# Kernel tuning notes

Hardware: AMD Instinct MI355X
Metric: run time of the kernel (lower is better)

The kernel has to match this reference:

```python
import jax, jax.numpy as jnp
import numpy as np
import math

B, H, N, D = 4, 8, 2048, 64


def setup_inputs() -> dict:
    key = jax.random.key(0)
    kq, kk, kv = jax.random.split(key, 3)
    q = jax.random.normal(kq, (B, H, N, D), dtype=jnp.float32)
    k = jax.random.normal(kk, (B, H, N, D), dtype=jnp.float32)
    v = jax.random.normal(kv, (B, H, N, D), dtype=jnp.float32)
    return {"q": q, "k": k, "v": v}


def reference(q, k, v):
    # global_attention_Sub: expanded squared L2 distance ||q_i - k_j||^2
    # = qq_i - 2 q_i.k_j + kk_j, then softmax(-dist/sqrt(D)) @ v.
    scale = math.sqrt(q.shape[-1])
    inner = -2.0 * jnp.einsum('bhnd,bhmd->bhnm', q, k)          # [B,H,N,N]
    qq = jnp.sum(q * q, axis=-1, keepdims=True)                  # [B,H,N,1]
    kk = jnp.sum(k * k, axis=-1, keepdims=True)                  # [B,H,N,1]
    diff_sq = qq + inner + jnp.swapaxes(kk, -1, -2)              # [B,H,N,N]
    attn = jax.nn.softmax(-diff_sq / scale, axis=-1)
    x = jnp.einsum('bhnm,bhmd->bhnd', attn, v)                   # [B,H,N,D]
    return jnp.transpose(x, (0, 2, 1, 3))                        # [B,N,H,D]
```

## Files before the change

### kernel.cpp

```cpp
#include <hip/hip_runtime.h>

typedef __bf16 bf16x4 __attribute__((ext_vector_type(4)));
typedef __bf16 bf16x8 __attribute__((ext_vector_type(8)));
typedef float floatx4 __attribute__((ext_vector_type(4)));

constexpr int Bc = 4, Hc = 8, Nc = 2048, Dc = 64;
constexpr int BQ = 128;
constexpr int WQ = 32;
constexpr int TK = 64;
constexpr int SKS = 72;
constexpr int SPS = 72;

__global__ __launch_bounds__(256, 2) void attn_dist_kernel(
    const float* __restrict__ Qg, const float* __restrict__ Kg,
    const float* __restrict__ Vg, float* __restrict__ Og)
{
    __shared__ __align__(16) __bf16 sK[TK * SKS];
    __shared__ __align__(16) __bf16 sV[Dc * 64];
    __shared__ __align__(16) __bf16 sP[BQ * SPS];
    __shared__ __align__(16) float  skk[TK];
    __shared__ __align__(16) float  sl[BQ];

    const int tid  = threadIdx.x;
    const int wave = tid >> 6;
    const int lane = tid & 63;
    const int qd   = lane >> 4;
    const int c    = lane & 15;

    const int qt = blockIdx.x;
    const int bh = blockIdx.y;
    const size_t base = (size_t)bh * Nc * Dc;
    const float* Qp = Qg + base;
    const float* Kp = Kg + base;
    const float* Vp = Vg + base;

    constexpr float LOG2E = 1.44269504088896340736f;
    const float qscale  = 0.25f  * LOG2E;
    const float kkscale = 0.125f * LOG2E;

    const int i0 = qt * BQ + wave * WQ;

    bf16x8 qf[2][2];
#pragma unroll
    for (int h = 0; h < 2; ++h) {
        const float* qrow = Qp + (size_t)(i0 + h * 16 + c) * Dc + qd * 8;
#pragma unroll
        for (int ks = 0; ks < 2; ++ks) {
            float4 a = *(const float4*)(qrow + ks * 32);
            float4 b = *(const float4*)(qrow + ks * 32 + 4);
            bf16x8 f;
            f[0] = (__bf16)(a.x * qscale); f[1] = (__bf16)(a.y * qscale);
            f[2] = (__bf16)(a.z * qscale); f[3] = (__bf16)(a.w * qscale);
            f[4] = (__bf16)(b.x * qscale); f[5] = (__bf16)(b.y * qscale);
            f[6] = (__bf16)(b.z * qscale); f[7] = (__bf16)(b.w * qscale);
            qf[h][ks] = f;
        }
    }

    const int js  = tid >> 2;
    const int ds_ = (tid & 3) * 16;

    float4 kreg[4], vreg[4];
    {
        const float* kr = Kp + (size_t)js * Dc + ds_;
        const float* vr = Vp + (size_t)js * Dc + ds_;
#pragma unroll
        for (int m = 0; m < 4; ++m) {
            kreg[m] = *(const float4*)(kr + m * 4);
            vreg[m] = *(const float4*)(vr + m * 4);
        }
    }

    floatx4 oacc[2][4];
#pragma unroll
    for (int h = 0; h < 2; ++h)
#pragma unroll
        for (int dt = 0; dt < 4; ++dt)
#pragma unroll
            for (int e = 0; e < 4; ++e) oacc[h][dt][e] = 0.f;
    float lp[2] = {0.f, 0.f};

    for (int jt = 0; jt < Nc / TK; ++jt) {
        __syncthreads();
        {
            float ss = 0.f;
#pragma unroll
            for (int m = 0; m < 4; ++m)
                ss += kreg[m].x * kreg[m].x + kreg[m].y * kreg[m].y
                    + kreg[m].z * kreg[m].z + kreg[m].w * kreg[m].w;
            ss += __shfl_xor(ss, 1);
            ss += __shfl_xor(ss, 2);
            if ((tid & 3) == 0) skk[js] = ss * kkscale;

            bf16x8 kb0, kb1;
            kb0[0]=(__bf16)kreg[0].x; kb0[1]=(__bf16)kreg[0].y;
            kb0[2]=(__bf16)kreg[0].z; kb0[3]=(__bf16)kreg[0].w;
            kb0[4]=(__bf16)kreg[1].x; kb0[5]=(__bf16)kreg[1].y;
            kb0[6]=(__bf16)kreg[1].z; kb0[7]=(__bf16)kreg[1].w;
            kb1[0]=(__bf16)kreg[2].x; kb1[1]=(__bf16)kreg[2].y;
            kb1[2]=(__bf16)kreg[2].z; kb1[3]=(__bf16)kreg[2].w;
            kb1[4]=(__bf16)kreg[3].x; kb1[5]=(__bf16)kreg[3].y;
            kb1[6]=(__bf16)kreg[3].z; kb1[7]=(__bf16)kreg[3].w;
            *(bf16x8*)&sK[js * SKS + ds_]     = kb0;
            *(bf16x8*)&sK[js * SKS + ds_ + 8] = kb1;

            float vv[16];
#pragma unroll
            for (int m = 0; m < 4; ++m) {
                vv[4*m+0] = vreg[m].x; vv[4*m+1] = vreg[m].y;
                vv[4*m+2] = vreg[m].z; vv[4*m+3] = vreg[m].w;
            }
            const int jc = js >> 3, jo = js & 7;
#pragma unroll
            for (int e = 0; e < 16; ++e) {
                const int d = ds_ + e;
                const int f = (d ^ (d >> 3)) & 7;
                sV[d * 64 + ((jc ^ f) << 3) + jo] = (__bf16)vv[e];
            }
        }
        __syncthreads();

        if (jt + 1 < Nc / TK) {
            const float* kr = Kp + (size_t)((jt + 1) * TK + js) * Dc + ds_;
            const float* vr = Vp + (size_t)((jt + 1) * TK + js) * Dc + ds_;
#pragma unroll
            for (int m = 0; m < 4; ++m) {
                kreg[m] = *(const float4*)(kr + m * 4);
                vreg[m] = *(const float4*)(vr + m * 4);
            }
        }

        floatx4 st[2][4];
#pragma unroll
        for (int kt = 0; kt < 4; ++kt) {
            floatx4 kkf = *(const floatx4*)&skk[kt * 16 + qd * 4];
#pragma unroll
            for (int r = 0; r < 4; ++r) { st[0][kt][r] = -kkf[r]; st[1][kt][r] = -kkf[r]; }
        }
#pragma unroll
        for (int kt = 0; kt < 4; ++kt)
#pragma unroll
            for (int ks = 0; ks < 2; ++ks) {
                bf16x8 kf = *(const bf16x8*)&sK[(kt * 16 + c) * SKS + ks * 32 + qd * 8];
                st[0][kt] = __builtin_amdgcn_mfma_f32_16x16x32_bf16(kf, qf[0][ks], st[0][kt], 0, 0, 0);
                st[1][kt] = __builtin_amdgcn_mfma_f32_16x16x32_bf16(kf, qf[1][ks], st[1][kt], 0, 0, 0);
            }

#pragma unroll
        for (int h = 0; h < 2; ++h) {
            const int prow = wave * WQ + h * 16 + c;
#pragma unroll
            for (int kt = 0; kt < 4; ++kt) {
                float p0 = __builtin_amdgcn_exp2f(st[h][kt][0]);
                float p1 = __builtin_amdgcn_exp2f(st[h][kt][1]);
                float p2 = __builtin_amdgcn_exp2f(st[h][kt][2]);
                float p3 = __builtin_amdgcn_exp2f(st[h][kt][3]);
                lp[h] += (p0 + p1) + (p2 + p3);
                bf16x4 pk;
                pk[0]=(__bf16)p0; pk[1]=(__bf16)p1; pk[2]=(__bf16)p2; pk[3]=(__bf16)p3;
                *(bf16x4*)&sP[prow * SPS + kt * 16 + qd * 4] = pk;
            }
        }

        bf16x8 pf[2][2];
#pragma unroll
        for (int h = 0; h < 2; ++h)
#pragma unroll
            for (int ks = 0; ks < 2; ++ks)
                pf[h][ks] = *(const bf16x8*)&sP[(wave * WQ + h * 16 + c) * SPS + ks * 32 + qd * 8];

#pragma unroll
        for (int dt = 0; dt < 4; ++dt) {
            const int d = dt * 16 + c;
            const int f = (d ^ (d >> 3)) & 7;
#pragma unroll
            for (int ks = 0; ks < 2; ++ks) {
                bf16x8 vf = *(const bf16x8*)&sV[d * 64 + (((ks * 4 + qd) ^ f) << 3)];
                oacc[0][dt] = __builtin_amdgcn_mfma_f32_16x16x32_bf16(pf[0][ks], vf, oacc[0][dt], 0, 0, 0);
                oacc[1][dt] = __builtin_amdgcn_mfma_f32_16x16x32_bf16(pf[1][ks], vf, oacc[1][dt], 0, 0, 0);
            }
        }
    }

#pragma unroll
    for (int h = 0; h < 2; ++h) {
        float l = lp[h];
        l += __shfl_xor(l, 16);
        l += __shfl_xor(l, 32);
        if (qd == 0) sl[wave * WQ + h * 16 + c] = l;
    }
    const int b = bh >> 3, hh = bh & 7;
#pragma unroll
    for (int h = 0; h < 2; ++h) {
        floatx4 lf = *(const floatx4*)&sl[wave * WQ + h * 16 + qd * 4];
#pragma unroll
        for (int r = 0; r < 4; ++r) {
            const float inv = 1.f / lf[r];
            const int i = i0 + h * 16 + qd * 4 + r;
            float* orow = Og + (((size_t)b * Nc + i) * Hc + hh) * Dc + c;
#pragma unroll
            for (int dt = 0; dt < 4; ++dt)
                orow[dt * 16] = oacc[h][dt][r] * inv;
        }
    }
}

extern "C" void kernel_launch(void* const* d_in, const int* in_sizes, int n_in,
                              void* d_out, int out_size, void* d_ws, size_t ws_size,
                              hipStream_t stream) {
    const float* q = (const float*)d_in[0];
    const float* k = (const float*)d_in[1];
    const float* v = (const float*)d_in[2];
    float* out = (float*)d_out;
    dim3 grid(Nc / BQ, Bc * Hc);
    dim3 block(256);
    attn_dist_kernel<<<grid, block, 0, stream>>>(q, k, v, out);
}
```

Before: 147.6 us.

## Precompute swizzled bf16 K/V tiles in workspace and stream them via global_load_lds

A prep kernel converts K and V once to bf16 and writes pre-swizzled tiles to the workspace: K in row-major swizzled form, V transposed. It also stores the negated, scaled squared K norms. The attention kernel then double-buffers tiles into LDS with direct global-to-LDS DMA and needs one barrier per iteration instead of two. This removes the per-block conversion, norm computation and scattered LDS stores that every query tile repeated. In exchange it adds a second launch and a workspace write/read pass, and relies on the async DMA being complete at the barrier.

```diff
diff --git a/kernel.cpp b/kernel.cpp
--- a/kernel.cpp
+++ b/kernel.cpp
@@ -8,17 +8,88 @@
 constexpr int BQ = 128;
 constexpr int WQ = 32;
 constexpr int TK = 64;
-constexpr int SKS = 72;
+constexpr int NT = Nc / TK;
 constexpr int SPS = 72;
-
-__global__ __launch_bounds__(256, 2) void attn_dist_kernel(
-    const float* __restrict__ Qg, const float* __restrict__ Kg,
-    const float* __restrict__ Vg, float* __restrict__ Og)
+constexpr float LOG2E = 1.44269504088896340736f;
+
+constexpr size_t KSW_OFF = 0;
+constexpr size_t VSW_OFF = (size_t)32 * NT * 8192;
+constexpr size_t KKN_OFF = VSW_OFF * 2;
+
+typedef __attribute__((address_space(1))) const unsigned int gu32;
+typedef __attribute__((address_space(3))) unsigned int lu32;
+__device__ __forceinline__ void dma16(const void* g, void* l) {
+    __builtin_amdgcn_global_load_lds((gu32*)g, (lu32*)l, 16, 0, 0);
+}
+__device__ __forceinline__ void dma4(const void* g, void* l) {
+    __builtin_amdgcn_global_load_lds((gu32*)g, (lu32*)l, 4, 0, 0);
+}
+
+__global__ __launch_bounds__(256) void prep_kernel(
+    const float* __restrict__ Kg, const float* __restrict__ Vg, char* __restrict__ ws)
 {
-    __shared__ __align__(16) __bf16 sK[TK * SKS];
-    __shared__ __align__(16) __bf16 sV[Dc * 64];
+    __shared__ float sT[64 * 68];
+    const int tid = threadIdx.x;
+    const int jt = blockIdx.x, bh = blockIdx.y;
+    const int js = tid >> 2, dc = tid & 3, ds_ = dc * 16;
+
+    __bf16* Ksw = (__bf16*)(ws + KSW_OFF);
+    __bf16* Vsw = (__bf16*)(ws + VSW_OFF);
+    float*  kkn = (float*)(ws + KKN_OFF);
+    const size_t rb = ((size_t)bh * Nc + jt * 64 + js) * Dc + ds_;
+
+    {
+        float4 a0 = *(const float4*)(Kg + rb);
+        float4 a1 = *(const float4*)(Kg + rb + 4);
+        float4 a2 = *(const float4*)(Kg + rb + 8);
+        float4 a3 = *(const float4*)(Kg + rb + 12);
+        float ss = a0.x*a0.x + a0.y*a0.y + a0.z*a0.z + a0.w*a0.w
+                 + a1.x*a1.x + a1.y*a1.y + a1.z*a1.z + a1.w*a1.w
+                 + a2.x*a2.x + a2.y*a2.y + a2.z*a2.z + a2.w*a2.w
+                 + a3.x*a3.x + a3.y*a3.y + a3.z*a3.z + a3.w*a3.w;
+        ss += __shfl_xor(ss, 1);
+        ss += __shfl_xor(ss, 2);
+        if (dc == 0) kkn[(size_t)bh * Nc + jt * 64 + js] = -(ss * 0.125f * LOG2E);
+        bf16x8 c0, c1;
+        c0[0]=(__bf16)a0.x; c0[1]=(__bf16)a0.y; c0[2]=(__bf16)a0.z; c0[3]=(__bf16)a0.w;
+        c0[4]=(__bf16)a1.x; c0[5]=(__bf16)a1.y; c0[6]=(__bf16)a1.z; c0[7]=(__bf16)a1.w;
+        c1[0]=(__bf16)a2.x; c1[1]=(__bf16)a2.y; c1[2]=(__bf16)a2.z; c1[3]=(__bf16)a2.w;
+        c1[4]=(__bf16)a3.x; c1[5]=(__bf16)a3.y; c1[6]=(__bf16)a3.z; c1[7]=(__bf16)a3.w;
+        __bf16* tile = Ksw + ((size_t)bh * NT + jt) * 4096;
+        *(bf16x8*)(tile + (js * 8 + ((dc * 2    ) ^ (js & 7))) * 8) = c0;
+        *(bf16x8*)(tile + (js * 8 + ((dc * 2 + 1) ^ (js & 7))) * 8) = c1;
+    }
+    {
+        float4 v0 = *(const float4*)(Vg + rb);
+        float4 v1 = *(const float4*)(Vg + rb + 4);
+        float4 v2 = *(const float4*)(Vg + rb + 8);
+        float4 v3 = *(const float4*)(Vg + rb + 12);
+        float* r = &sT[js * 68 + ds_];
+        *(float4*)r = v0; *(float4*)(r + 4) = v1;
+        *(float4*)(r + 8) = v2; *(float4*)(r + 12) = v3;
+    }
+    __syncthreads();
+    {
+        const int d = tid >> 2;
+        __bf16* tile = Vsw + ((size_t)bh * NT + jt) * 4096;
+#pragma unroll
+        for (int e2 = 0; e2 < 2; ++e2) {
+            const int kc = (tid & 3) * 2 + e2;
+            bf16x8 cc;
+#pragma unroll
+            for (int e = 0; e < 8; ++e) cc[e] = (__bf16)sT[(kc * 8 + e) * 68 + d];
+            *(bf16x8*)(tile + (d * 8 + (kc ^ (d & 7))) * 8) = cc;
+        }
+    }
+}
+
+__global__ __launch_bounds__(256, 2) void attn_kernel(
+    const float* __restrict__ Qg, const char* __restrict__ ws, float* __restrict__ Og)
+{
+    __shared__ __align__(16) __bf16 sK[2][4096];
+    __shared__ __align__(16) __bf16 sV[2][4096];
+    __shared__ __align__(16) float  skk[2][64];
     __shared__ __align__(16) __bf16 sP[BQ * SPS];
-    __shared__ __align__(16) float  skk[TK];
     __shared__ __align__(16) float  sl[BQ];
 
     const int tid  = threadIdx.x;
@@ -29,21 +100,18 @@
 
     const int qt = blockIdx.x;
     const int bh = blockIdx.y;
-    const size_t base = (size_t)bh * Nc * Dc;
-    const float* Qp = Qg + base;
-    const float* Kp = Kg + base;
-    const float* Vp = Vg + base;
-
-    constexpr float LOG2E = 1.44269504088896340736f;
-    const float qscale  = 0.25f  * LOG2E;
-    const float kkscale = 0.125f * LOG2E;
-
+
+    const char* Kimg = ws + KSW_OFF + (size_t)bh * NT * 8192;
+    const char* Vimg = ws + VSW_OFF + (size_t)bh * NT * 8192;
+    const float* kkp = (const float*)(ws + KKN_OFF) + (size_t)bh * Nc;
+
+    const float qscale = 0.25f * LOG2E;
     const int i0 = qt * BQ + wave * WQ;
 
     bf16x8 qf[2][2];
 #pragma unroll
     for (int h = 0; h < 2; ++h) {
-        const float* qrow = Qp + (size_t)(i0 + h * 16 + c) * Dc + qd * 8;
+        const float* qrow = Qg + ((size_t)bh * Nc + i0 + h * 16 + c) * Dc + qd * 8;
 #pragma unroll
         for (int ks = 0; ks < 2; ++ks) {
             float4 a = *(const float4*)(qrow + ks * 32);
@@ -57,19 +125,8 @@
         }
     }
 
-    const int js  = tid >> 2;
-    const int ds_ = (tid & 3) * 16;
-
-    float4 kreg[4], vreg[4];
-    {
-        const float* kr = Kp + (size_t)js * Dc + ds_;
-        const float* vr = Vp + (size_t)js * Dc + ds_;
-#pragma unroll
-        for (int m = 0; m < 4; ++m) {
-            kreg[m] = *(const float4*)(kr + m * 4);
-            vreg[m] = *(const float4*)(vr + m * 4);
-        }
-    }
+    const int koff0 = c * 64 + ((qd ^ (c & 7)) << 3);
+    const int koff1 = c * 64 + (((4 + qd) ^ (c & 7)) << 3);
 
     floatx4 oacc[2][4];
 #pragma unroll
@@ -80,71 +137,42 @@
             for (int e = 0; e < 4; ++e) oacc[h][dt][e] = 0.f;
     float lp[2] = {0.f, 0.f};
 
-    for (int jt = 0; jt < Nc / TK; ++jt) {
+    auto stage = [&](int jt, int b) {
+        const char* ki = Kimg + (size_t)jt * 8192;
+        const char* vi = Vimg + (size_t)jt * 8192;
+#pragma unroll
+        for (int i = 0; i < 2; ++i) {
+            const int off    = wave * 2048 + i * 1024 + lane * 16;
+            const int ldsoff = wave * 2048 + i * 1024;
+            dma16(ki + off, (char*)&sK[b][0] + ldsoff);
+            dma16(vi + off, (char*)&sV[b][0] + ldsoff);
+        }
+        if (wave == 3) dma4(kkp + jt * 64 + lane, &skk[b][0]);
+    };
+
+    stage(0, 0);
+
+    for (int jt = 0; jt < NT; ++jt) {
+        const int b = jt & 1;
         __syncthreads();
-        {
-            float ss = 0.f;
-#pragma unroll
-            for (int m = 0; m < 4; ++m)
-                ss += kreg[m].x * kreg[m].x + kreg[m].y * kreg[m].y
-                    + kreg[m].z * kreg[m].z + kreg[m].w * kreg[m].w;
-            ss += __shfl_xor(ss, 1);
-            ss += __shfl_xor(ss, 2);
-            if ((tid & 3) == 0) skk[js] = ss * kkscale;
-
-            bf16x8 kb0, kb1;
-            kb0[0]=(__bf16)kreg[0].x; kb0[1]=(__bf16)kreg[0].y;
-            kb0[2]=(__bf16)kreg[0].z; kb0[3]=(__bf16)kreg[0].w;
-            kb0[4]=(__bf16)kreg[1].x; kb0[5]=(__bf16)kreg[1].y;
-            kb0[6]=(__bf16)kreg[1].z; kb0[7]=(__bf16)kreg[1].w;
-            kb1[0]=(__bf16)kreg[2].x; kb1[1]=(__bf16)kreg[2].y;
-            kb1[2]=(__bf16)kreg[2].z; kb1[3]=(__bf16)kreg[2].w;
-            kb1[4]=(__bf16)kreg[3].x; kb1[5]=(__bf16)kreg[3].y;
-            kb1[6]=(__bf16)kreg[3].z; kb1[7]=(__bf16)kreg[3].w;
-            *(bf16x8*)&sK[js * SKS + ds_]     = kb0;
-            *(bf16x8*)&sK[js * SKS + ds_ + 8] = kb1;
-
-            float vv[16];
-#pragma unroll
-            for (int m = 0; m < 4; ++m) {
-                vv[4*m+0] = vreg[m].x; vv[4*m+1] = vreg[m].y;
-                vv[4*m+2] = vreg[m].z; vv[4*m+3] = vreg[m].w;
-            }
-            const int jc = js >> 3, jo = js & 7;
-#pragma unroll
-            for (int e = 0; e < 16; ++e) {
-                const int d = ds_ + e;
-                const int f = (d ^ (d >> 3)) & 7;
-                sV[d * 64 + ((jc ^ f) << 3) + jo] = (__bf16)vv[e];
-            }
-        }
-        __syncthreads();
-
-        if (jt + 1 < Nc / TK) {
-            const float* kr = Kp + (size_t)((jt + 1) * TK + js) * Dc + ds_;
-            const float* vr = Vp + (size_t)((jt + 1) * TK + js) * Dc + ds_;
-#pragma unroll
-            for (int m = 0; m < 4; ++m) {
-                kreg[m] = *(const float4*)(kr + m * 4);
-                vreg[m] = *(const float4*)(vr + m * 4);
-            }
-        }
+        if (jt + 1 < NT) stage(jt + 1, b ^ 1);
 
         floatx4 st[2][4];
 #pragma unroll
         for (int kt = 0; kt < 4; ++kt) {
-            floatx4 kkf = *(const floatx4*)&skk[kt * 16 + qd * 4];
-#pragma unroll
-            for (int r = 0; r < 4; ++r) { st[0][kt][r] = -kkf[r]; st[1][kt][r] = -kkf[r]; }
-        }
-#pragma unroll
-        for (int kt = 0; kt < 4; ++kt)
-#pragma unroll
-            for (int ks = 0; ks < 2; ++ks) {
-                bf16x8 kf = *(const bf16x8*)&sK[(kt * 16 + c) * SKS + ks * 32 + qd * 8];
-                st[0][kt] = __builtin_amdgcn_mfma_f32_16x16x32_bf16(kf, qf[0][ks], st[0][kt], 0, 0, 0);
-                st[1][kt] = __builtin_amdgcn_mfma_f32_16x16x32_bf16(kf, qf[1][ks], st[1][kt], 0, 0, 0);
-            }
+            floatx4 kkf = *(const floatx4*)&skk[b][kt * 16 + qd * 4];
+            st[0][kt] = kkf; st[1][kt] = kkf;
+        }
+#pragma unroll
+        for (int kt = 0; kt < 4; ++kt) {
+            const __bf16* kbase = &sK[b][kt * 1024];
+            bf16x8 kf0 = *(const bf16x8*)(kbase + koff0);
+            bf16x8 kf1 = *(const bf16x8*)(kbase + koff1);
+            st[0][kt] = __builtin_amdgcn_mfma_f32_16x16x32_bf16(kf0, qf[0][0], st[0][kt], 0, 0, 0);
+            st[0][kt] = __builtin_amdgcn_mfma_f32_16x16x32_bf16(kf1, qf[0][1], st[0][kt], 0, 0, 0);
+            st[1][kt] = __builtin_amdgcn_mfma_f32_16x16x32_bf16(kf0, qf[1][0], st[1][kt], 0, 0, 0);
+            st[1][kt] = __builtin_amdgcn_mfma_f32_16x16x32_bf16(kf1, qf[1][1], st[1][kt], 0, 0, 0);
+        }
 
 #pragma unroll
         for (int h = 0; h < 2; ++h) {
@@ -157,11 +185,11 @@
                 float p3 = __builtin_amdgcn_exp2f(st[h][kt][3]);
                 lp[h] += (p0 + p1) + (p2 + p3);
                 bf16x4 pk;
-                pk[0]=(__bf16)p0; pk[1]=(__bf16)p1; pk[2]=(__bf16)p2; pk[3]=(__bf16)p3;
+                pk[0] = (__bf16)p0; pk[1] = (__bf16)p1;
+                pk[2] = (__bf16)p2; pk[3] = (__bf16)p3;
                 *(bf16x4*)&sP[prow * SPS + kt * 16 + qd * 4] = pk;
             }
         }
-
         bf16x8 pf[2][2];
 #pragma unroll
         for (int h = 0; h < 2; ++h)
@@ -171,14 +199,13 @@
 
 #pragma unroll
         for (int dt = 0; dt < 4; ++dt) {
-            const int d = dt * 16 + c;
-            const int f = (d ^ (d >> 3)) & 7;
-#pragma unroll
-            for (int ks = 0; ks < 2; ++ks) {
-                bf16x8 vf = *(const bf16x8*)&sV[d * 64 + (((ks * 4 + qd) ^ f) << 3)];
-                oacc[0][dt] = __builtin_amdgcn_mfma_f32_16x16x32_bf16(pf[0][ks], vf, oacc[0][dt], 0, 0, 0);
-                oacc[1][dt] = __builtin_amdgcn_mfma_f32_16x16x32_bf16(pf[1][ks], vf, oacc[1][dt], 0, 0, 0);
-            }
+            const __bf16* vbase = &sV[b][dt * 1024];
+            bf16x8 vf0 = *(const bf16x8*)(vbase + koff0);
+            bf16x8 vf1 = *(const bf16x8*)(vbase + koff1);
+            oacc[0][dt] = __builtin_amdgcn_mfma_f32_16x16x32_bf16(pf[0][0], vf0, oacc[0][dt], 0, 0, 0);
+            oacc[0][dt] = __builtin_amdgcn_mfma_f32_16x16x32_bf16(pf[0][1], vf1, oacc[0][dt], 0, 0, 0);
+            oacc[1][dt] = __builtin_amdgcn_mfma_f32_16x16x32_bf16(pf[1][0], vf0, oacc[1][dt], 0, 0, 0);
+            oacc[1][dt] = __builtin_amdgcn_mfma_f32_16x16x32_bf16(pf[1][1], vf1, oacc[1][dt], 0, 0, 0);
         }
     }
 
@@ -189,7 +216,7 @@
         l += __shfl_xor(l, 32);
         if (qd == 0) sl[wave * WQ + h * 16 + c] = l;
     }
-    const int b = bh >> 3, hh = bh & 7;
+    const int b_ = bh >> 3, hh = bh & 7;
 #pragma unroll
     for (int h = 0; h < 2; ++h) {
         floatx4 lf = *(const floatx4*)&sl[wave * WQ + h * 16 + qd * 4];
@@ -197,7 +224,7 @@
         for (int r = 0; r < 4; ++r) {
             const float inv = 1.f / lf[r];
             const int i = i0 + h * 16 + qd * 4 + r;
-            float* orow = Og + (((size_t)b * Nc + i) * Hc + hh) * Dc + c;
+            float* orow = Og + (((size_t)b_ * Nc + i) * Hc + hh) * Dc + c;
 #pragma unroll
             for (int dt = 0; dt < 4; ++dt)
                 orow[dt * 16] = oacc[h][dt][r] * inv;
@@ -212,7 +239,7 @@
     const float* k = (const float*)d_in[1];
     const float* v = (const float*)d_in[2];
     float* out = (float*)d_out;
-    dim3 grid(Nc / BQ, Bc * Hc);
-    dim3 block(256);
-    attn_dist_kernel<<<grid, block, 0, stream>>>(q, k, v, out);
-}
+    char* ws = (char*)d_ws;
+    prep_kernel<<<dim3(NT, Bc * Hc), 256, 0, stream>>>(k, v, ws);
+    attn_kernel<<<dim3(Nc / BQ, Bc * Hc), 256, 0, stream>>>(q, ws, out);
+}
```

Result: faster. 140.8 us (-4.6%).
